# Optimization experiments

Measured on AMD Instinct MI355X. Metric: run time of the kernel, lower is better.

The kernel has to match this reference:

```python
import jax, jax.numpy as jnp
import numpy as np

N = 100000          # num nodes
K = 50              # num sampled neighbors per node (num_samples)
F_IN = 128          # in_features
F_OUT = 128         # out_features


def setup_inputs() -> dict:
    key = jax.random.key(0)
    k1, k2, k3, k4 = jax.random.split(key, 4)
    x = jax.random.normal(k1, (N, F_IN), dtype=jnp.float32)
    neighbors = jax.random.randint(k2, (N, K), 0, N, dtype=jnp.int64)
    stdv = 1.0 / np.sqrt(F_OUT)
    weight = jax.random.uniform(k3, (2 * F_IN, F_OUT), dtype=jnp.float32,
                                minval=-stdv, maxval=stdv)
    bias = jax.random.uniform(k4, (F_OUT,), dtype=jnp.float32,
                              minval=-stdv, maxval=stdv)
    return {"x": x, "neighbors": neighbors, "weight": weight, "bias": bias}


def reference(x, neighbors, weight, bias):
    # aggregate: gather sampled neighbor features and mean-reduce (aggregator='mean')
    # x[neighbors]: [N, K, F_IN] -> mean over K -> [N, F_IN]
    agg = jnp.mean(jnp.take(x, neighbors, axis=0), axis=1)
    # concat self + aggregated, linear, bias, relu
    h = jnp.concatenate([x, agg], axis=1)  # [N, 2*F_IN]
    out = h @ weight + bias                # [N, F_OUT]
    return jax.nn.relu(out)
```

## Files before the change

### kernel.cpp

```cpp
#include <hip/hip_runtime.h>
#include <hip/hip_bf16.h>
#include <stdint.h>

#define NN 100000
#define KN 50
#define FIN 128
#define FOUT 128
#define BM 64

typedef __attribute__((ext_vector_type(8))) short bf16x8;
typedef __attribute__((ext_vector_type(4))) float f32x4;
typedef __attribute__((ext_vector_type(2))) float f32x2;

__device__ __forceinline__ uint16_t f2b(float f){
  uint32_t x = __builtin_bit_cast(uint32_t, f);
  x += 0x7fffu + ((x >> 16) & 1u);
  return (uint16_t)(x >> 16);
}

__global__ void cast_fp8_kernel(const float* __restrict__ x, uint32_t* __restrict__ xf8){
  int i = blockIdx.x * blockDim.x + threadIdx.x;
  float4 v = *(const float4*)(x + (size_t)i * 4);
  uint32_t p = 0;
  p = __builtin_amdgcn_cvt_pk_fp8_f32(v.x, v.y, p, false);
  p = __builtin_amdgcn_cvt_pk_fp8_f32(v.z, v.w, p, true);
  xf8[i] = p;
}

__global__ void pack_w_kernel(const float* __restrict__ w, uint16_t* __restrict__ wp){
  int kt = blockIdx.x >> 3, nt = blockIdx.x & 7;
  int lane = threadIdx.x;
  int col = nt * 16 + (lane & 15);
  int k0  = kt * 32 + ((lane >> 4) << 3);
  uint16_t vals[8];
  #pragma unroll
  for (int i = 0; i < 8; i++) vals[i] = f2b(w[(k0 + i) * FOUT + col]);
  *(uint4*)(wp + ((size_t)(kt * 8 + nt) * 64 + lane) * 8) = *(const uint4*)vals;
}

__global__ void detect_kernel(const int* __restrict__ nb, int* __restrict__ flag){
  int i = blockIdx.x * blockDim.x + threadIdx.x;
  if (nb[2 * i + 1] != 0) *flag = 1;
}

__global__ __launch_bounds__(256) void gather_kernel(
    const uint8_t* __restrict__ xf8,
    const int* __restrict__ nbrs,
    const int* __restrict__ flag,
    uint16_t* __restrict__ agg)
{
  __shared__ int idxs[4][8 * KN];
  const int tid  = threadIdx.x;
  const int wave = tid >> 6, lane = tid & 63;
  const int base = blockIdx.x * 32;
  const int stride_mul = (*flag != 0) ? 1 : 2;

  {
    long long fb = (long long)(base + wave * 8) * KN;
    #pragma unroll
    for (int t = lane; t < 8 * KN; t += 64)
      idxs[wave][t] = nbrs[(fb + t) * stride_mul];
  }
  __syncthreads();

  const int g  = lane >> 3;
  const int fl = (lane & 7) * 16;
  const int node = base + wave * 8 + g;
  const int* ip = &idxs[wave][g * KN];

  f32x2 acc[8];
  #pragma unroll
  for (int i = 0; i < 8; i++) acc[i] = (f32x2){0.f, 0.f};

  #pragma unroll 10
  for (int k = 0; k < KN; k++){
    int j = ip[k];
    uint4 v = *(const uint4*)(xf8 + ((size_t)(uint32_t)j << 7) + fl);
    acc[0] += __builtin_amdgcn_cvt_pk_f32_fp8(v.x, false);
    acc[1] += __builtin_amdgcn_cvt_pk_f32_fp8(v.x, true);
    acc[2] += __builtin_amdgcn_cvt_pk_f32_fp8(v.y, false);
    acc[3] += __builtin_amdgcn_cvt_pk_f32_fp8(v.y, true);
    acc[4] += __builtin_amdgcn_cvt_pk_f32_fp8(v.z, false);
    acc[5] += __builtin_amdgcn_cvt_pk_f32_fp8(v.z, true);
    acc[6] += __builtin_amdgcn_cvt_pk_f32_fp8(v.w, false);
    acc[7] += __builtin_amdgcn_cvt_pk_f32_fp8(v.w, true);
  }

  uint16_t o[16];
  #pragma unroll
  for (int i = 0; i < 8; i++){
    o[2*i]   = f2b(acc[i].x * (1.0f / KN));
    o[2*i+1] = f2b(acc[i].y * (1.0f / KN));
  }
  uint16_t* dst = agg + (size_t)node * FIN + fl;
  *(uint4*)(dst)     = *(const uint4*)(o);
  *(uint4*)(dst + 8) = *(const uint4*)(o + 8);
}

__global__ __launch_bounds__(256) void gemm_kernel(
    const float* __restrict__ x,
    const uint16_t* __restrict__ agg,
    const uint16_t* __restrict__ wp,
    const float* __restrict__ bias,
    float* __restrict__ out)
{
  __shared__ uint16_t h[BM][264];
  const int tid  = threadIdx.x;
  const int wave = tid >> 6, lane = tid & 63;
  const int base = blockIdx.x * BM;

  #pragma unroll
  for (int jj = 0; jj < 8; jj++){
    int ci = jj * 256 + tid;
    int r = ci >> 5, c = ci & 31;
    int node = base + r; if (node >= NN) node = NN - 1;
    float4 v = *(const float4*)(x + (size_t)node * FIN + c * 4);
    ushort4 o2; o2.x = f2b(v.x); o2.y = f2b(v.y); o2.z = f2b(v.z); o2.w = f2b(v.w);
    *(ushort4*)(&h[r][c * 4]) = o2;
  }
  #pragma unroll
  for (int jj = 0; jj < 4; jj++){
    int ci = jj * 256 + tid;
    int r = ci >> 4, c = ci & 15;
    int node = base + r; if (node >= NN) node = NN - 1;
    uint4 v = *(const uint4*)(agg + (size_t)node * FIN + c * 8);
    *(uint4*)(&h[r][FIN + c * 8]) = v;
  }

  bf16x8 bfr[8][2];
  #pragma unroll
  for (int kt = 0; kt < 8; kt++)
    #pragma unroll
    for (int ntl = 0; ntl < 2; ntl++){
      int nt = wave * 2 + ntl;
      bfr[kt][ntl] = *(const bf16x8*)(wp + ((size_t)(kt * 8 + nt) * 64 + lane) * 8);
    }

  __syncthreads();

  f32x4 acc[4][2];
  #pragma unroll
  for (int mt = 0; mt < 4; mt++)
    for (int n = 0; n < 2; n++) acc[mt][n] = (f32x4){0.f, 0.f, 0.f, 0.f};

  const int arow = lane & 15;
  const int ak   = (lane >> 4) << 3;
  #pragma unroll
  for (int kt = 0; kt < 8; kt++){
    #pragma unroll
    for (int mt = 0; mt < 4; mt++){
      bf16x8 af = *(const bf16x8*)(&h[mt * 16 + arow][kt * 32 + ak]);
      acc[mt][0] = __builtin_amdgcn_mfma_f32_16x16x32_bf16(af, bfr[kt][0], acc[mt][0], 0, 0, 0);
      acc[mt][1] = __builtin_amdgcn_mfma_f32_16x16x32_bf16(af, bfr[kt][1], acc[mt][1], 0, 0, 0);
    }
  }

  #pragma unroll
  for (int ntl = 0; ntl < 2; ntl++){
    int col = wave * 32 + ntl * 16 + (lane & 15);
    float bv = bias[col];
    #pragma unroll
    for (int mt = 0; mt < 4; mt++){
      #pragma unroll
      for (int i = 0; i < 4; i++){
        int row = mt * 16 + ((lane >> 4) << 2) + i;
        int node = base + row;
        if (node < NN){
          float v = acc[mt][ntl][i] + bv;
          out[(size_t)node * FOUT + col] = fmaxf(v, 0.f);
        }
      }
    }
  }
}

extern "C" void kernel_launch(void* const* d_in, const int* in_sizes, int n_in,
                              void* d_out, int out_size, void* d_ws, size_t ws_size,
                              hipStream_t stream){
  const float* x    = (const float*)d_in[0];
  const int*   nbrs = (const int*)d_in[1];
  const float* w    = (const float*)d_in[2];
  const float* bias = (const float*)d_in[3];
  float* out = (float*)d_out;

  uint8_t*  xf8  = (uint8_t*)d_ws;
  uint16_t* wp   = (uint16_t*)((char*)d_ws + (size_t)NN * FIN);
  int*      flag = (int*)((char*)d_ws + (size_t)NN * FIN + 65536);
  uint16_t* agg  = (uint16_t*)((char*)d_ws + (size_t)NN * FIN + 131072);

  (void)hipMemsetAsync(flag, 0, 4, stream);
  cast_fp8_kernel<<<NN * FIN / 4 / 256, 256, 0, stream>>>(x, (uint32_t*)xf8);
  pack_w_kernel<<<64, 64, 0, stream>>>(w, wp);
  detect_kernel<<<32, 256, 0, stream>>>(nbrs, flag);
  gather_kernel<<<NN / 32, 256, 0, stream>>>(xf8, nbrs, flag, agg);
  gemm_kernel<<<(NN + BM - 1) / BM, 256, 0, stream>>>(x, agg, wp, bias, out);
}
```

Baseline: 123.3 us.

## Partition gather by feature panel per XCD pair to improve L2 locality

The gather kernel now splits the 128-byte fp8 feature row into four 32-byte panels. Each panel is assigned to a pair of XCDs via the block index, so each XCD's L2 only caches a quarter of the feature table. Each block handles 128 nodes, and each pair of lanes covers one node's 32-byte panel. In exchange, the neighbor indices are loaded four times, once per panel, and each gather request is narrower.

```diff
diff --git a/kernel.cpp b/kernel.cpp
--- a/kernel.cpp
+++ b/kernel.cpp
@@ -7,6 +7,8 @@
 #define FIN 128
 #define FOUT 128
 #define BM 64
+#define PBLK 128
+#define NCHUNK 782
 
 typedef __attribute__((ext_vector_type(8))) short bf16x8;
 typedef __attribute__((ext_vector_type(4))) float f32x4;
@@ -49,24 +51,27 @@
     const int* __restrict__ flag,
     uint16_t* __restrict__ agg)
 {
-  __shared__ int idxs[4][8 * KN];
+  __shared__ int idxs[PBLK][51];
   const int tid  = threadIdx.x;
   const int wave = tid >> 6, lane = tid & 63;
-  const int base = blockIdx.x * 32;
+  const int b    = blockIdx.x;
+  const int xcd  = b & 7;
+  const int panel = xcd >> 1;
+  const int chunk = ((b >> 3) << 1) + (xcd & 1);
+  const int base  = chunk * PBLK;
   const int stride_mul = (*flag != 0) ? 1 : 2;
 
-  {
-    long long fb = (long long)(base + wave * 8) * KN;
-    #pragma unroll
-    for (int t = lane; t < 8 * KN; t += 64)
-      idxs[wave][t] = nbrs[(fb + t) * stride_mul];
+  for (int t = tid; t < PBLK * KN; t += 256){
+    int r = t / KN, c = t - r * KN;
+    int node = base + r; if (node >= NN) node = NN - 1;
+    idxs[r][c] = nbrs[(node * KN + c) * stride_mul];
   }
   __syncthreads();
 
-  const int g  = lane >> 3;
-  const int fl = (lane & 7) * 16;
-  const int node = base + wave * 8 + g;
-  const int* ip = &idxs[wave][g * KN];
+  const int r    = (wave << 5) + (lane >> 1);
+  const int half = lane & 1;
+  const int foff = panel * 32 + half * 16;
+  const int* ip  = &idxs[r][0];
 
   f32x2 acc[8];
   #pragma unroll
@@ -75,7 +80,7 @@
   #pragma unroll 10
   for (int k = 0; k < KN; k++){
     int j = ip[k];
-    uint4 v = *(const uint4*)(xf8 + ((size_t)(uint32_t)j << 7) + fl);
+    uint4 v = *(const uint4*)(xf8 + ((size_t)(uint32_t)j << 7) + foff);
     acc[0] += __builtin_amdgcn_cvt_pk_f32_fp8(v.x, false);
     acc[1] += __builtin_amdgcn_cvt_pk_f32_fp8(v.x, true);
     acc[2] += __builtin_amdgcn_cvt_pk_f32_fp8(v.y, false);
@@ -86,15 +91,18 @@
     acc[7] += __builtin_amdgcn_cvt_pk_f32_fp8(v.w, true);
   }
 
-  uint16_t o[16];
-  #pragma unroll
-  for (int i = 0; i < 8; i++){
-    o[2*i]   = f2b(acc[i].x * (1.0f / KN));
-    o[2*i+1] = f2b(acc[i].y * (1.0f / KN));
-  }
-  uint16_t* dst = agg + (size_t)node * FIN + fl;
-  *(uint4*)(dst)     = *(const uint4*)(o);
-  *(uint4*)(dst + 8) = *(const uint4*)(o + 8);
+  const int node = base + r;
+  if (node < NN){
+    uint16_t o[16];
+    #pragma unroll
+    for (int i = 0; i < 8; i++){
+      o[2*i]   = f2b(acc[i].x * (1.0f / KN));
+      o[2*i+1] = f2b(acc[i].y * (1.0f / KN));
+    }
+    uint16_t* dst = agg + (size_t)node * FIN + panel * 32 + half * 16;
+    *(uint4*)(dst)     = *(const uint4*)(o);
+    *(uint4*)(dst + 8) = *(const uint4*)(o + 8);
+  }
 }
 
 __global__ __launch_bounds__(256) void gemm_kernel(
@@ -192,6 +200,6 @@
   cast_fp8_kernel<<<NN * FIN / 4 / 256, 256, 0, stream>>>(x, (uint32_t*)xf8);
   pack_w_kernel<<<64, 64, 0, stream>>>(w, wp);
   detect_kernel<<<32, 256, 0, stream>>>(nbrs, flag);
-  gather_kernel<<<NN / 32, 256, 0, stream>>>(xf8, nbrs, flag, agg);
+  gather_kernel<<<NCHUNK * 4, 256, 0, stream>>>(xf8, nbrs, flag, agg);
   gemm_kernel<<<(NN + BM - 1) / BM, 256, 0, stream>>>(x, agg, wp, bias, out);
 }
```

After: 308.8 us. +150.5%, slower.

## Bin neighbor indices by node range and sweep bins with grid-wide barrier

Applied to the files above, without the earlier changes.

Gather is restructured so each block handles 128 rows and sorts each row's neighbor indices into four node-range bins in shared memory. All blocks then process bin 0, meet at a software grid barrier built on a global atomic counter, and move on to the next bin. The goal is to keep the active slice of the fp8 feature table resident in cache during each phase. The cost is extra sorting work, lower parallelism (782 blocks), and a spin barrier with an iteration cap that could deadlock or silently time out if not all blocks are co-resident.

```diff
diff --git a/kernel.cpp b/kernel.cpp
--- a/kernel.cpp
+++ b/kernel.cpp
@@ -7,6 +7,10 @@
 #define FIN 128
 #define FOUT 128
 #define BM 64
+#define NB 782
+#define RPB 128
+#define NBIN 4
+#define BINSZ 25000
 
 typedef __attribute__((ext_vector_type(8))) short bf16x8;
 typedef __attribute__((ext_vector_type(4))) float f32x4;
@@ -43,58 +47,118 @@
   if (nb[2 * i + 1] != 0) *flag = 1;
 }
 
-__global__ __launch_bounds__(256) void gather_kernel(
+#define CVT8(ACC, v)                                           \
+  ACC[0] += __builtin_amdgcn_cvt_pk_f32_fp8((v).x, false);     \
+  ACC[1] += __builtin_amdgcn_cvt_pk_f32_fp8((v).x, true);      \
+  ACC[2] += __builtin_amdgcn_cvt_pk_f32_fp8((v).y, false);     \
+  ACC[3] += __builtin_amdgcn_cvt_pk_f32_fp8((v).y, true);      \
+  ACC[4] += __builtin_amdgcn_cvt_pk_f32_fp8((v).z, false);     \
+  ACC[5] += __builtin_amdgcn_cvt_pk_f32_fp8((v).z, true);      \
+  ACC[6] += __builtin_amdgcn_cvt_pk_f32_fp8((v).w, false);     \
+  ACC[7] += __builtin_amdgcn_cvt_pk_f32_fp8((v).w, true);
+
+#define PASS_ROW(ACC, RR) {                                              \
+  int r = (wave << 5) + ((RR) << 3) + g;                                 \
+  int k0 = off[r][p], k1 = off[r][p + 1];                                \
+  for (int k = k0; k < k1; ++k){                                         \
+    int j = srt[r][k];                                                   \
+    uint4 v = *(const uint4*)(xf8 + ((size_t)(uint32_t)j << 7) + fl);    \
+    CVT8(ACC, v);                                                        \
+  } }
+
+#define STORE_ROW(ACC, RR) {                                             \
+  int r = (wave << 5) + ((RR) << 3) + g;                                 \
+  int node = base + r;                                                   \
+  if (node < NN){                                                        \
+    uint16_t o[16];                                                      \
+    _Pragma("unroll")                                                    \
+    for (int i = 0; i < 8; i++){                                         \
+      o[2*i]   = f2b(ACC[i].x * (1.0f / KN));                            \
+      o[2*i+1] = f2b(ACC[i].y * (1.0f / KN));                            \
+    }                                                                    \
+    uint16_t* dst = agg + (size_t)node * FIN + fl;                       \
+    *(uint4*)(dst)     = *(const uint4*)(o);                             \
+    *(uint4*)(dst + 8) = *(const uint4*)(o + 8);                         \
+  } }
+
+__global__ __launch_bounds__(256, 4) void gather_kernel(
     const uint8_t* __restrict__ xf8,
     const int* __restrict__ nbrs,
     const int* __restrict__ flag,
-    uint16_t* __restrict__ agg)
+    uint16_t* __restrict__ agg,
+    int* __restrict__ bar)
 {
-  __shared__ int idxs[4][8 * KN];
+  __shared__ int    srt[RPB][KN];
+  __shared__ int    cnt[RPB][NBIN];
+  __shared__ ushort off[RPB][NBIN + 1];
   const int tid  = threadIdx.x;
   const int wave = tid >> 6, lane = tid & 63;
-  const int base = blockIdx.x * 32;
-  const int stride_mul = (*flag != 0) ? 1 : 2;
-
-  {
-    long long fb = (long long)(base + wave * 8) * KN;
-    #pragma unroll
-    for (int t = lane; t < 8 * KN; t += 64)
-      idxs[wave][t] = nbrs[(fb + t) * stride_mul];
+  const int base = blockIdx.x * RPB;
+  const int sm = (*flag != 0) ? 1 : 2;
+
+  for (int t = tid; t < RPB * NBIN; t += 256) ((int*)cnt)[t] = 0;
+  __syncthreads();
+
+  for (int e = tid; e < RPB * KN; e += 256){
+    int r = e / KN, c = e - r * KN;
+    int node = base + r; if (node >= NN) node = NN - 1;
+    int j = nbrs[(node * KN + c) * sm];
+    atomicAdd(&cnt[r][j / BINSZ], 1);
+  }
+  __syncthreads();
+  if (tid < RPB){
+    int s = 0;
+    #pragma unroll
+    for (int p = 0; p < NBIN; ++p){ off[tid][p] = (ushort)s; s += cnt[tid][p]; }
+    off[tid][NBIN] = (ushort)s;
+  }
+  __syncthreads();
+  if (tid < RPB){
+    int node = base + tid; if (node >= NN) node = NN - 1;
+    unsigned long long cur = 0;
+    #pragma unroll
+    for (int p = 0; p < NBIN; ++p)
+      cur |= (unsigned long long)off[tid][p] << (16 * p);
+    for (int k = 0; k < KN; ++k){
+      int j = nbrs[(node * KN + k) * sm];
+      int b = j / BINSZ;
+      int pos = (int)((cur >> (16 * b)) & 0xffffULL);
+      cur += 1ULL << (16 * b);
+      srt[tid][pos] = j;
+    }
   }
   __syncthreads();
 
   const int g  = lane >> 3;
   const int fl = (lane & 7) * 16;
-  const int node = base + wave * 8 + g;
-  const int* ip = &idxs[wave][g * KN];
-
-  f32x2 acc[8];
-  #pragma unroll
-  for (int i = 0; i < 8; i++) acc[i] = (f32x2){0.f, 0.f};
-
-  #pragma unroll 10
-  for (int k = 0; k < KN; k++){
-    int j = ip[k];
-    uint4 v = *(const uint4*)(xf8 + ((size_t)(uint32_t)j << 7) + fl);
-    acc[0] += __builtin_amdgcn_cvt_pk_f32_fp8(v.x, false);
-    acc[1] += __builtin_amdgcn_cvt_pk_f32_fp8(v.x, true);
-    acc[2] += __builtin_amdgcn_cvt_pk_f32_fp8(v.y, false);
-    acc[3] += __builtin_amdgcn_cvt_pk_f32_fp8(v.y, true);
-    acc[4] += __builtin_amdgcn_cvt_pk_f32_fp8(v.z, false);
-    acc[5] += __builtin_amdgcn_cvt_pk_f32_fp8(v.z, true);
-    acc[6] += __builtin_amdgcn_cvt_pk_f32_fp8(v.w, false);
-    acc[7] += __builtin_amdgcn_cvt_pk_f32_fp8(v.w, true);
-  }
-
-  uint16_t o[16];
+  f32x2 acc0[8], acc1[8], acc2[8], acc3[8];
   #pragma unroll
   for (int i = 0; i < 8; i++){
-    o[2*i]   = f2b(acc[i].x * (1.0f / KN));
-    o[2*i+1] = f2b(acc[i].y * (1.0f / KN));
-  }
-  uint16_t* dst = agg + (size_t)node * FIN + fl;
-  *(uint4*)(dst)     = *(const uint4*)(o);
-  *(uint4*)(dst + 8) = *(const uint4*)(o + 8);
+    acc0[i] = (f32x2){0.f, 0.f}; acc1[i] = (f32x2){0.f, 0.f};
+    acc2[i] = (f32x2){0.f, 0.f}; acc3[i] = (f32x2){0.f, 0.f};
+  }
+
+  for (int p = 0; p < NBIN; ++p){
+    if (p){
+      __syncthreads();
+      if (tid == 0){
+        atomicAdd(bar, 1);
+        int tgt = NB * p, it = 0;
+        while (__hip_atomic_load(bar, __ATOMIC_RELAXED, __HIP_MEMORY_SCOPE_AGENT) < tgt
+               && it < 20000){ __builtin_amdgcn_s_sleep(1); ++it; }
+      }
+      __syncthreads();
+    }
+    PASS_ROW(acc0, 0)
+    PASS_ROW(acc1, 1)
+    PASS_ROW(acc2, 2)
+    PASS_ROW(acc3, 3)
+  }
+
+  STORE_ROW(acc0, 0)
+  STORE_ROW(acc1, 1)
+  STORE_ROW(acc2, 2)
+  STORE_ROW(acc3, 3)
 }
 
 __global__ __launch_bounds__(256) void gemm_kernel(
@@ -186,12 +250,13 @@
   uint8_t*  xf8  = (uint8_t*)d_ws;
   uint16_t* wp   = (uint16_t*)((char*)d_ws + (size_t)NN * FIN);
   int*      flag = (int*)((char*)d_ws + (size_t)NN * FIN + 65536);
+  int*      bar  = flag + 1;
   uint16_t* agg  = (uint16_t*)((char*)d_ws + (size_t)NN * FIN + 131072);
 
-  (void)hipMemsetAsync(flag, 0, 4, stream);
+  (void)hipMemsetAsync(flag, 0, 8, stream);
   cast_fp8_kernel<<<NN * FIN / 4 / 256, 256, 0, stream>>>(x, (uint32_t*)xf8);
   pack_w_kernel<<<64, 64, 0, stream>>>(w, wp);
   detect_kernel<<<32, 256, 0, stream>>>(nbrs, flag);
-  gather_kernel<<<NN / 32, 256, 0, stream>>>(xf8, nbrs, flag, agg);
+  gather_kernel<<<NB, 256, 0, stream>>>(xf8, nbrs, flag, agg, bar);
   gemm_kernel<<<(NN + BM - 1) / BM, 256, 0, stream>>>(x, agg, wp, bias, out);
 }
```

New measurement: 318.6 us. 158% more time.
